# Kernel tuning notes

Hardware: AMD Instinct MI355X
Metric: run time of the kernel (lower is better)

Reference implementation:

```python
import jax, jax.numpy as jnp
import numpy as np

N_E = 1024
E_DIM = 256
N_TOK = 65536
BETA = 0.25


def setup_inputs() -> dict:
    key = jax.random.key(0)
    k1, k2 = jax.random.split(key)
    z = jax.random.normal(k1, (N_TOK, E_DIM), dtype=jnp.float32)
    # nn.Embedding weight, init uniform(-1/n_e, 1/n_e) in the original; use normal-like scale via uniform
    W = jax.random.uniform(k2, (N_E, E_DIM), dtype=jnp.float32, minval=-1.0 / N_E, maxval=1.0 / N_E)
    return {"z": z, "W": W}


def reference(z, W):
    # cosine distance: d = -normalize(z) @ normalize(W).T  -> (N, n_e)
    zn = z / jnp.linalg.norm(z, axis=-1, keepdims=True)
    Wn = W / jnp.linalg.norm(W, axis=-1, keepdims=True)
    d = -jnp.einsum('nd,ed->ne', zn, Wn)
    min_idx = jnp.argmin(d, axis=1)                       # (N,)
    z_q = W[min_idx]                                       # (N, e_dim)
    # commitment / codebook loss with straight-through style detaches
    loss = jnp.mean((jax.lax.stop_gradient(z) - z_q) ** 2) \
         + BETA * jnp.mean((z - jax.lax.stop_gradient(z_q)) ** 2)
    # pos_indices = unique(min_idx) (sorted); neg = np.delete(arange(n_e), pos) (sorted)
    # emb = cat(W[pos], W[neg]); reproduce with a stable argsort on membership mask
    pos_mask = jnp.zeros((N_E,), dtype=bool).at[min_idx].set(True)
    order = jnp.argsort(jnp.logical_not(pos_mask), stable=True)  # pos (sorted) first, then neg (sorted)
    emb = W[order]                                         # (n_e, e_dim)
    label = pos_mask[order].astype(z.dtype)                # (n_e,)
    return emb, label, loss
```

## Files before the change

kernel.cpp:

```cpp
#include <hip/hip_runtime.h>
#include <math.h>


typedef unsigned short u16;
typedef unsigned int   u32;
typedef __attribute__((ext_vector_type(8))) short short8;
typedef __attribute__((ext_vector_type(4))) float f32x4;

#define N_E   1024
#define E_DIM 256
#define N_TOK 65536
#define BETA  0.25f
#define CAP   16
#define D_ADM 0.08f
#define D_FIL 0.09f

#define WS_INVNORM 0
#define WS_MASK    4096
#define WS_LACC    12288
#define WS_WSW     16384
#define WS_CNT     540672
#define WS_CAND    802816

static __device__ __forceinline__ u16 f2bf(float f) {
    u32 u = __float_as_uint(f);
    u32 r = (u + 0x7FFFu + ((u >> 16) & 1u)) >> 16;
    return (u16)r;
}
static __device__ __forceinline__ u32 keyenc(float f) {
    u32 u = __float_as_uint(f);
    return u ^ (u32)(((int)u >> 31) | 0x80000000);
}
static __device__ __forceinline__ float keydec(u32 k) {
    u32 u = (k & 0x80000000u) ? (k ^ 0x80000000u) : ~k;
    return __uint_as_float(u);
}

__global__ void k_prep(const float* __restrict__ W, u16* __restrict__ Wsw,
                       float* __restrict__ inv_norm, int* __restrict__ mask,
                       double* __restrict__ lacc) {
    const int n = blockIdx.x;
    const int l = threadIdx.x;
    const float4 v = reinterpret_cast<const float4*>(W + (size_t)n * E_DIM)[l];
    float s = v.x * v.x + v.y * v.y + v.z * v.z + v.w * v.w;
#pragma unroll
    for (int sh = 1; sh < 64; sh <<= 1) s += __shfl_xor(s, sh, 64);
    const float inv = 1.0f / sqrtf(s);
    if (l == 0) {
        inv_norm[n] = inv;
        mask[n] = 0;
        if (n < 256) lacc[n] = 0.0;
    }
    const int o = l >> 1;
    const int kc = o >> 2, q = o & 3;
    const size_t base =
        (((((size_t)(n >> 7) * 8 + kc) * 8 + ((n >> 4) & 7)) * 64 +
          (q * 16 + (n & 15))) * 8) + (l & 1) * 4;
    u16* dst = Wsw + base;
    dst[0] = f2bf(v.x * inv);
    dst[1] = f2bf(v.y * inv);
    dst[2] = f2bf(v.z * inv);
    dst[3] = f2bf(v.w * inv);
}

__global__ __launch_bounds__(512, 4)
void k_score(const float* __restrict__ z, const u16* __restrict__ Wsw,
             u16* __restrict__ cand_g, u32* __restrict__ cnt_g) {
    __shared__ u16 A_sw[32768];
    __shared__ u32 bestk[128];
    __shared__ u32 cnt[128];
    __shared__ u32 slots[128 * CAP];

    const int t    = threadIdx.x;
    const int lane = t & 63;
    const int w    = t >> 6;
    const int mq2  = w >> 1;
    const int nq   = w & 1;
    const size_t tok_base = (size_t)blockIdx.x * 128;

    if (t < 128) { bestk[t] = 0u; cnt[t] = 0u; }

#pragma unroll
    for (int i = 0; i < 8; i++) {
        const int c = t + 512 * i;
        const int m = c >> 5, o = c & 31;
        const float* zp = z + (tok_base + m) * E_DIM + o * 8;
        const float4 v0 = reinterpret_cast<const float4*>(zp)[0];
        const float4 v1 = reinterpret_cast<const float4*>(zp)[1];
        uint4 d;
        d.x = (u32)f2bf(v0.x) | ((u32)f2bf(v0.y) << 16);
        d.y = (u32)f2bf(v0.z) | ((u32)f2bf(v0.w) << 16);
        d.z = (u32)f2bf(v1.x) | ((u32)f2bf(v1.y) << 16);
        d.w = (u32)f2bf(v1.z) | ((u32)f2bf(v1.w) << 16);
        const int kc = o >> 2, q = o & 3, col = m & 15, mt = m >> 4;
        *reinterpret_cast<uint4*>(A_sw + ((size_t)((kc * 8 + mt) * 64 + q * 16 + col)) * 8) = d;
    }
    __syncthreads();

    const int q   = lane >> 4;
    const int col = lane & 15;
    const u16* wb = Wsw + (size_t)(nq * 4) * 512 + (size_t)lane * 8;

#pragma unroll 1
    for (int nb = 0; nb < 8; nb++) {
        f32x4 acc[2][4];
#pragma unroll
        for (int mi = 0; mi < 2; mi++)
#pragma unroll
            for (int ni = 0; ni < 4; ni++) {
                f32x4 zf = {0.f, 0.f, 0.f, 0.f};
                acc[mi][ni] = zf;
            }

#pragma unroll 2
        for (int kc = 0; kc < 8; kc++) {
            short8 bf[4], af[2];
#pragma unroll
            for (int ni = 0; ni < 4; ni++)
                bf[ni] = *reinterpret_cast<const short8*>(
                    wb + (size_t)(nb * 64 + kc * 8 + ni) * 512);
#pragma unroll
            for (int mi = 0; mi < 2; mi++)
                af[mi] = *reinterpret_cast<const short8*>(
                    A_sw + ((size_t)((kc * 8 + mq2 * 2 + mi) * 64 + lane)) * 8);
#pragma unroll
            for (int mi = 0; mi < 2; mi++)
#pragma unroll
                for (int ni = 0; ni < 4; ni++)
                    acc[mi][ni] = __builtin_amdgcn_mfma_f32_16x16x32_bf16(
                        af[mi], bf[ni], acc[mi][ni], 0, 0, 0);
        }

#pragma unroll
        for (int mi = 0; mi < 2; mi++)
#pragma unroll
            for (int r = 0; r < 4; r++) {
                float m0 = fmaxf(fmaxf(acc[mi][0][r], acc[mi][1][r]),
                                 fmaxf(acc[mi][2][r], acc[mi][3][r]));
#pragma unroll
                for (int sh = 1; sh < 16; sh <<= 1)
                    m0 = fmaxf(m0, __shfl_xor(m0, sh, 64));
                if (col == 0)
                    atomicMax(&bestk[mq2 * 32 + mi * 16 + q * 4 + r], keyenc(m0));
            }
        __syncthreads();

        float thr[8];
#pragma unroll
        for (int mi = 0; mi < 2; mi++)
#pragma unroll
            for (int r = 0; r < 4; r++)
                thr[mi * 4 + r] = keydec(bestk[mq2 * 32 + mi * 16 + q * 4 + r]) - D_ADM;

#pragma unroll
        for (int mi = 0; mi < 2; mi++)
#pragma unroll
            for (int ni = 0; ni < 4; ni++)
#pragma unroll
                for (int r = 0; r < 4; r++) {
                    const float v = acc[mi][ni][r];
                    if (v >= thr[mi * 4 + r]) {
                        const int tok  = mq2 * 32 + mi * 16 + q * 4 + r;
                        const int code = nb * 128 + nq * 64 + ni * 16 + col;
                        const u32 slot = atomicAdd(&cnt[tok], 1u);
                        if (slot < CAP) {
                            const float vc = fminf(fmaxf((v + 16.0f) * 1024.0f, 0.0f), 65535.0f);
                            slots[tok * CAP + slot] = ((u32)vc << 16) | (u32)code;
                        }
                    }
                }
    }

    __syncthreads();
    if (t < 128) {
        const size_t tokg = tok_base + t;
        const u32 c = cnt[t];
        if (c > CAP) {
            cnt_g[tokg] = 0xFFFFFFFFu;
        } else {
            const float thrf = keydec(bestk[t]) - D_FIL;
            u32 m = 0;
            for (u32 i = 0; i < c; i++) {
                const u32 s = slots[t * CAP + i];
                const float approx = (float)(s >> 16) * (1.0f / 1024.0f) - 16.0f;
                if (approx >= thrf) cand_g[tokg * 16 + (m++)] = (u16)(s & 0xFFFFu);
            }
            cnt_g[tokg] = m;
        }
    }
}

__global__ __launch_bounds__(256)
void k_pick(const float* __restrict__ z, const float* __restrict__ W,
            const float* __restrict__ inv_norm, const u16* __restrict__ cand_g,
            const u32* __restrict__ cnt_g, int* __restrict__ mask,
            double* __restrict__ lacc) {
    const int t    = threadIdx.x;
    const int lane = t & 63;
    const int w    = t >> 6;
    const int gl   = t & 15;
    const int grp  = t >> 4;
    const size_t tok = (size_t)blockIdx.x * 16 + grp;

    float4 zv[4];
#pragma unroll
    for (int j = 0; j < 4; j++)
        zv[j] = reinterpret_cast<const float4*>(z + tok * E_DIM)[j * 16 + gl];

    const u32 sc = cnt_g[tok];
    int bi;
    if (sc == 1u) {
        bi = cand_g[tok * 16];
    } else {
        float bv = -3.4e38f;
        bi = 0x7FFFFFFF;
        const bool full = (sc == 0xFFFFFFFFu);
        const int n_it = full ? N_E : (int)sc;
#pragma unroll 1
        for (int i = 0; i < n_it; i++) {
            const int c = full ? i : (int)cand_g[tok * 16 + i];
            float p = 0.f;
#pragma unroll
            for (int j = 0; j < 4; j++) {
                const float4 wv = reinterpret_cast<const float4*>(W + (size_t)c * E_DIM)[j * 16 + gl];
                p += zv[j].x * wv.x + zv[j].y * wv.y + zv[j].z * wv.z + zv[j].w * wv.w;
            }
#pragma unroll
            for (int sh = 1; sh < 16; sh <<= 1) p += __shfl_xor(p, sh, 64);
            const float s = p * inv_norm[c];
            if (s > bv || (s == bv && c < bi)) { bv = s; bi = c; }
        }
    }

    float lsum = 0.f;
#pragma unroll
    for (int j = 0; j < 4; j++) {
        const float4 wv = reinterpret_cast<const float4*>(W + (size_t)bi * E_DIM)[j * 16 + gl];
        const float dx = zv[j].x - wv.x, dy = zv[j].y - wv.y;
        const float dz2 = zv[j].z - wv.z, dw = zv[j].w - wv.w;
        lsum += dx * dx + dy * dy + dz2 * dz2 + dw * dw;
    }
    if (gl == 0) mask[bi] = 1;

#pragma unroll
    for (int sh = 1; sh < 64; sh <<= 1) lsum += __shfl_xor(lsum, sh, 64);
    if (lane == 0) atomicAdd(&lacc[(blockIdx.x * 4 + w) & 255], (double)lsum);
}

__global__ __launch_bounds__(256)
void k_emit(const float* __restrict__ W, const int* __restrict__ mask,
            const double* __restrict__ lacc, float* __restrict__ out) {
    __shared__ int   redp[256], redt[256];
    __shared__ double dred[256];
    const int e = blockIdx.x;
    const int t = threadIdx.x;
    const int4 mv = reinterpret_cast<const int4*>(mask)[t];
    const int b = t * 4;
    redt[t] = mv.x + mv.y + mv.z + mv.w;
    redp[t] = (b + 0 < e ? mv.x : 0) + (b + 1 < e ? mv.y : 0) +
              (b + 2 < e ? mv.z : 0) + (b + 3 < e ? mv.w : 0);
    if (e == 0) dred[t] = lacc[t];
    __syncthreads();
#pragma unroll
    for (int s2 = 128; s2 > 0; s2 >>= 1) {
        if (t < s2) {
            redp[t] += redp[t + s2];
            redt[t] += redt[t + s2];
            if (e == 0) dred[t] += dred[t + s2];
        }
        __syncthreads();
    }
    const int prefix = redp[0], total = redt[0];
    const int m = mask[e];
    const int r = m ? prefix : (total + e - prefix);
    out[(size_t)r * E_DIM + t] = W[(size_t)e * E_DIM + t];
    if (t == 0) out[(size_t)N_E * E_DIM + r] = m ? 1.0f : 0.0f;
    if (e == 0 && t == 0) {
        const double mse = dred[0] / (double)((size_t)N_TOK * E_DIM);
        out[(size_t)N_E * E_DIM + N_E] = (float)((1.0 + (double)BETA) * mse);
    }
}

extern "C" void kernel_launch(void* const* d_in, const int* in_sizes, int n_in,
                              void* d_out, int out_size, void* d_ws, size_t ws_size,
                              hipStream_t stream) {
    const float* z = (const float*)d_in[0];
    const float* W = (const float*)d_in[1];
    float* out = (float*)d_out;
    char* ws = (char*)d_ws;

    float*  inv_norm = (float*)(ws + WS_INVNORM);
    int*    mask     = (int*)(ws + WS_MASK);
    double* lacc     = (double*)(ws + WS_LACC);
    u16*    Wsw      = (u16*)(ws + WS_WSW);
    u32*    cnt      = (u32*)(ws + WS_CNT);
    u16*    cand     = (u16*)(ws + WS_CAND);

    k_prep <<<N_E, 64, 0, stream>>>(W, Wsw, inv_norm, mask, lacc);
    k_score<<<N_TOK / 128, 512, 0, stream>>>(z, Wsw, cand, cnt);
    k_pick <<<N_TOK / 16, 256, 0, stream>>>(z, W, inv_norm, cand, cnt, mask, lacc);
    k_emit <<<N_E, 256, 0, stream>>>(W, mask, lacc, out);
}
```

Baseline: 161.8 us.

## Resolve unambiguous tokens in score kernel and compact ambiguous ones for pick

The score kernel now accumulates ||z||^2 during the bf16 staging and, when a token has a single surviving candidate, derives its squared-error term algebraically from the best cosine score and ||W|| while setting the mask directly. Only ambiguous tokens are appended to a compacted worklist, and a small persistent pick kernel processes that list. This removes the full second pass over z and W for most tokens. The MFMA loop is also restructured into a 4x2 tile with software-pipelined double-buffered fragment loads, and score quantisation is made finer. The loss now relies on a bf16-derived best score (approx error) and uses a smaller global candidate cap.

Measured after the change: 541.8 us. 235% more time.

```diff
diff --git a/kernel.cpp b/kernel.cpp
--- a/kernel.cpp
+++ b/kernel.cpp
@@ -4,6 +4,7 @@
 
 typedef unsigned short u16;
 typedef unsigned int   u32;
+typedef unsigned long long u64;
 typedef __attribute__((ext_vector_type(8))) short short8;
 typedef __attribute__((ext_vector_type(4))) float f32x4;
 
@@ -11,21 +12,24 @@
 #define E_DIM 256
 #define N_TOK 65536
 #define BETA  0.25f
-#define CAP   16
+#define CAPL  16
+#define CAPG  8
 #define D_ADM 0.08f
 #define D_FIL 0.09f
 
 #define WS_INVNORM 0
-#define WS_MASK    4096
+#define WS_NORMW   4096
+#define WS_MASK    8192
 #define WS_LACC    12288
+#define WS_WCNT    14336
 #define WS_WSW     16384
 #define WS_CNT     540672
 #define WS_CAND    802816
+#define WS_WLIST   1851392
 
 static __device__ __forceinline__ u16 f2bf(float f) {
     u32 u = __float_as_uint(f);
-    u32 r = (u + 0x7FFFu + ((u >> 16) & 1u)) >> 16;
-    return (u16)r;
+    return (u16)((u + 0x7FFFu + ((u >> 16) & 1u)) >> 16);
 }
 static __device__ __forceinline__ u32 keyenc(float f) {
     u32 u = __float_as_uint(f);
@@ -37,19 +41,20 @@
 }
 
 __global__ void k_prep(const float* __restrict__ W, u16* __restrict__ Wsw,
-                       float* __restrict__ inv_norm, int* __restrict__ mask,
-                       double* __restrict__ lacc) {
+                       float* __restrict__ inv_norm, float* __restrict__ normW,
+                       int* __restrict__ mask, double* __restrict__ lacc,
+                       u32* __restrict__ wcnt) {
     const int n = blockIdx.x;
     const int l = threadIdx.x;
     const float4 v = reinterpret_cast<const float4*>(W + (size_t)n * E_DIM)[l];
     float s = v.x * v.x + v.y * v.y + v.z * v.z + v.w * v.w;
 #pragma unroll
     for (int sh = 1; sh < 64; sh <<= 1) s += __shfl_xor(s, sh, 64);
-    const float inv = 1.0f / sqrtf(s);
+    const float nw = sqrtf(s), inv = 1.0f / nw;
     if (l == 0) {
-        inv_norm[n] = inv;
-        mask[n] = 0;
+        inv_norm[n] = inv; normW[n] = nw; mask[n] = 0;
         if (n < 256) lacc[n] = 0.0;
+        if (n == 0) *wcnt = 0u;
     }
     const int o = l >> 1;
     const int kc = o >> 2, q = o & 3;
@@ -65,160 +70,183 @@
 
 __global__ __launch_bounds__(512, 4)
 void k_score(const float* __restrict__ z, const u16* __restrict__ Wsw,
-             u16* __restrict__ cand_g, u32* __restrict__ cnt_g) {
-    __shared__ u16 A_sw[32768];
+             const float* __restrict__ normW, u16* __restrict__ cand_g,
+             u32* __restrict__ cnt_g, int* __restrict__ mask,
+             u32* __restrict__ wlist, u32* __restrict__ wcnt,
+             double* __restrict__ lacc) {
+    __shared__ __align__(16) u16 A_sw[32768];
     __shared__ u32 bestk[128];
     __shared__ u32 cnt[128];
-    __shared__ u32 slots[128 * CAP];
+    __shared__ u32 slots[128 * CAPL];
 
     const int t    = threadIdx.x;
     const int lane = t & 63;
     const int w    = t >> 6;
-    const int mq2  = w >> 1;
-    const int nq   = w & 1;
     const size_t tok_base = (size_t)blockIdx.x * 128;
 
     if (t < 128) { bestk[t] = 0u; cnt[t] = 0u; }
 
-#pragma unroll
-    for (int i = 0; i < 8; i++) {
-        const int c = t + 512 * i;
-        const int m = c >> 5, o = c & 31;
-        const float* zp = z + (tok_base + m) * E_DIM + o * 8;
-        const float4 v0 = reinterpret_cast<const float4*>(zp)[0];
-        const float4 v1 = reinterpret_cast<const float4*>(zp)[1];
-        uint4 d;
-        d.x = (u32)f2bf(v0.x) | ((u32)f2bf(v0.y) << 16);
-        d.y = (u32)f2bf(v0.z) | ((u32)f2bf(v0.w) << 16);
-        d.z = (u32)f2bf(v1.x) | ((u32)f2bf(v1.y) << 16);
-        d.w = (u32)f2bf(v1.z) | ((u32)f2bf(v1.w) << 16);
-        const int kc = o >> 2, q = o & 3, col = m & 15, mt = m >> 4;
-        *reinterpret_cast<uint4*>(A_sw + ((size_t)((kc * 8 + mt) * 64 + q * 16 + col)) * 8) = d;
-    }
+    float ssq = 0.f;
+    {
+        const int col16 = lane & 15, oq = lane >> 4;
+#pragma unroll
+        for (int i = 0; i < 8; i++) {
+            const int f  = i * 8 + w;
+            const int kc = f >> 3, mt = f & 7;
+            const int m  = mt * 16 + col16;
+            const int o  = kc * 4 + oq;
+            const float* zp = z + (tok_base + m) * E_DIM + o * 8;
+            const float4 v0 = reinterpret_cast<const float4*>(zp)[0];
+            const float4 v1 = reinterpret_cast<const float4*>(zp)[1];
+            ssq += v0.x * v0.x + v0.y * v0.y + v0.z * v0.z + v0.w * v0.w
+                 + v1.x * v1.x + v1.y * v1.y + v1.z * v1.z + v1.w * v1.w;
+            uint4 d;
+            d.x = (u32)f2bf(v0.x) | ((u32)f2bf(v0.y) << 16);
+            d.y = (u32)f2bf(v0.z) | ((u32)f2bf(v0.w) << 16);
+            d.z = (u32)f2bf(v1.x) | ((u32)f2bf(v1.y) << 16);
+            d.w = (u32)f2bf(v1.z) | ((u32)f2bf(v1.w) << 16);
+            *reinterpret_cast<uint4*>(A_sw + (size_t)f * 512 + (size_t)lane * 8) = d;
+        }
+    }
+#pragma unroll
+    for (int sh = 1; sh < 64; sh <<= 1) ssq += __shfl_xor(ssq, sh, 64);
+    if (lane == 0) atomicAdd(&lacc[(blockIdx.x * 8 + w) & 255], (double)ssq);
     __syncthreads();
 
-    const int q   = lane >> 4;
-    const int col = lane & 15;
-    const u16* wb = Wsw + (size_t)(nq * 4) * 512 + (size_t)lane * 8;
-
-#pragma unroll 1
-    for (int nb = 0; nb < 8; nb++) {
-        f32x4 acc[2][4];
-#pragma unroll
-        for (int mi = 0; mi < 2; mi++)
-#pragma unroll
-            for (int ni = 0; ni < 4; ni++) {
-                f32x4 zf = {0.f, 0.f, 0.f, 0.f};
-                acc[mi][ni] = zf;
-            }
-
-#pragma unroll 2
-        for (int kc = 0; kc < 8; kc++) {
-            short8 bf[4], af[2];
-#pragma unroll
-            for (int ni = 0; ni < 4; ni++)
-                bf[ni] = *reinterpret_cast<const short8*>(
-                    wb + (size_t)(nb * 64 + kc * 8 + ni) * 512);
-#pragma unroll
-            for (int mi = 0; mi < 2; mi++)
-                af[mi] = *reinterpret_cast<const short8*>(
-                    A_sw + ((size_t)((kc * 8 + mq2 * 2 + mi) * 64 + lane)) * 8);
-#pragma unroll
-            for (int mi = 0; mi < 2; mi++)
-#pragma unroll
-                for (int ni = 0; ni < 4; ni++)
-                    acc[mi][ni] = __builtin_amdgcn_mfma_f32_16x16x32_bf16(
-                        af[mi], bf[ni], acc[mi][ni], 0, 0, 0);
-        }
-
-#pragma unroll
-        for (int mi = 0; mi < 2; mi++)
-#pragma unroll
-            for (int r = 0; r < 4; r++) {
-                float m0 = fmaxf(fmaxf(acc[mi][0][r], acc[mi][1][r]),
-                                 fmaxf(acc[mi][2][r], acc[mi][3][r]));
-#pragma unroll
-                for (int sh = 1; sh < 16; sh <<= 1)
-                    m0 = fmaxf(m0, __shfl_xor(m0, sh, 64));
-                if (col == 0)
-                    atomicMax(&bestk[mq2 * 32 + mi * 16 + q * 4 + r], keyenc(m0));
-            }
-        __syncthreads();
-
-        float thr[8];
-#pragma unroll
-        for (int mi = 0; mi < 2; mi++)
-#pragma unroll
-            for (int r = 0; r < 4; r++)
-                thr[mi * 4 + r] = keydec(bestk[mq2 * 32 + mi * 16 + q * 4 + r]) - D_ADM;
-
-#pragma unroll
-        for (int mi = 0; mi < 2; mi++)
-#pragma unroll
-            for (int ni = 0; ni < 4; ni++)
+    const int mq = w >> 2;
+    const int nq = w & 3;
+    const int q = lane >> 4, col = lane & 15;
+    const u16* wbase = Wsw + (size_t)(nq * 2) * 512 + (size_t)lane * 8;
+
+    f32x4 acc[4][2];
+#pragma unroll
+    for (int mi = 0; mi < 4; mi++)
+#pragma unroll
+        for (int ni = 0; ni < 2; ni++) {
+            f32x4 zf = {0.f, 0.f, 0.f, 0.f};
+            acc[mi][ni] = zf;
+        }
+
+#define LOAD_B(S, D) { \
+    D[0] = *reinterpret_cast<const short8*>(wbase + (size_t)((S) * 8 + 0) * 512); \
+    D[1] = *reinterpret_cast<const short8*>(wbase + (size_t)((S) * 8 + 1) * 512); }
+#define LOAD_A(S, D) { const int _k8 = ((S) & 7) * 8; \
+    D[0] = *reinterpret_cast<const short8*>(A_sw + (size_t)(_k8 + mq * 4 + 0) * 512 + (size_t)lane * 8); \
+    D[1] = *reinterpret_cast<const short8*>(A_sw + (size_t)(_k8 + mq * 4 + 1) * 512 + (size_t)lane * 8); \
+    D[2] = *reinterpret_cast<const short8*>(A_sw + (size_t)(_k8 + mq * 4 + 2) * 512 + (size_t)lane * 8); \
+    D[3] = *reinterpret_cast<const short8*>(A_sw + (size_t)(_k8 + mq * 4 + 3) * 512 + (size_t)lane * 8); }
+#define MFMA_STEP(AF, BF) { \
+    _Pragma("unroll") for (int mi = 0; mi < 4; mi++) \
+    _Pragma("unroll") for (int ni = 0; ni < 2; ni++) \
+        acc[mi][ni] = __builtin_amdgcn_mfma_f32_16x16x32_bf16(AF[mi], BF[ni], acc[mi][ni], 0, 0, 0); }
+
+    short8 afc[4], bfc[2], afn[4], bfn[2];
+    LOAD_B(0, bfc); LOAD_A(0, afc);
+
+#pragma unroll 4
+    for (int s = 0; s < 64; s += 2) {
+        LOAD_B(s + 1, bfn); LOAD_A(s + 1, afn);
+        MFMA_STEP(afc, bfc);
+        if (s < 62) { LOAD_B(s + 2, bfc); LOAD_A(s + 2, afc); }
+        MFMA_STEP(afn, bfn);
+        if (((s + 1) & 7) == 7) {
+            const int nb = (s + 1) >> 3;
+#pragma unroll
+            for (int mi = 0; mi < 4; mi++)
 #pragma unroll
                 for (int r = 0; r < 4; r++) {
-                    const float v = acc[mi][ni][r];
-                    if (v >= thr[mi * 4 + r]) {
-                        const int tok  = mq2 * 32 + mi * 16 + q * 4 + r;
-                        const int code = nb * 128 + nq * 64 + ni * 16 + col;
-                        const u32 slot = atomicAdd(&cnt[tok], 1u);
-                        if (slot < CAP) {
-                            const float vc = fminf(fmaxf((v + 16.0f) * 1024.0f, 0.0f), 65535.0f);
-                            slots[tok * CAP + slot] = ((u32)vc << 16) | (u32)code;
+                    float m0 = fmaxf(acc[mi][0][r], acc[mi][1][r]);
+#pragma unroll
+                    for (int sh = 1; sh < 16; sh <<= 1)
+                        m0 = fmaxf(m0, __shfl_xor(m0, sh, 64));
+                    const int tk = mq * 64 + mi * 16 + q * 4 + r;
+                    if (col == 0) atomicMax(&bestk[tk], keyenc(m0));
+                    const float thr = fmaxf(m0, keydec(bestk[tk])) - D_ADM;
+#pragma unroll
+                    for (int ni = 0; ni < 2; ni++) {
+                        const float v = acc[mi][ni][r];
+                        if (v >= thr) {
+                            const int code = nb * 128 + nq * 32 + ni * 16 + col;
+                            const u32 sl = atomicAdd(&cnt[tk], 1u);
+                            if (sl < CAPL) {
+                                const float vc = fminf(fmaxf((v + 16.f) * 2048.f, 0.f), 65535.f);
+                                slots[tk * CAPL + sl] = ((u32)vc << 16) | (u32)code;
+                            }
                         }
+                        acc[mi][ni][r] = 0.f;
                     }
                 }
-    }
+        }
+    }
+#undef LOAD_B
+#undef LOAD_A
+#undef MFMA_STEP
 
     __syncthreads();
     if (t < 128) {
         const size_t tokg = tok_base + t;
         const u32 c = cnt[t];
-        if (c > CAP) {
-            cnt_g[tokg] = 0xFFFFFFFFu;
+        const float best = keydec(bestk[t]);
+        bool amb = false;
+        float xacc = 0.f;
+        if (c > CAPL) {
+            cnt_g[tokg] = 0xFFFFFFFFu; amb = true;
         } else {
-            const float thrf = keydec(bestk[t]) - D_FIL;
-            u32 m = 0;
+            const float thrf = best - D_FIL;
+            u16 loc[CAPG]; u32 m = 0;
             for (u32 i = 0; i < c; i++) {
-                const u32 s = slots[t * CAP + i];
-                const float approx = (float)(s >> 16) * (1.0f / 1024.0f) - 16.0f;
-                if (approx >= thrf) cand_g[tokg * 16 + (m++)] = (u16)(s & 0xFFFFu);
+                const u32 s2 = slots[t * CAPL + i];
+                const float ap = (float)(s2 >> 16) * (1.0f / 2048.0f) - 16.0f;
+                if (ap >= thrf) { if (m < CAPG) loc[m] = (u16)(s2 & 0xFFFFu); m++; }
             }
-            cnt_g[tokg] = m;
-        }
+            if (m == 1) {
+                const int bi = loc[0];
+                mask[bi] = 1;
+                const float nw = normW[bi];
+                xacc = fmaf(-2.0f * best, nw, nw * nw);
+            } else if (m <= CAPG) {
+                for (u32 i = 0; i < m; i++) cand_g[tokg * CAPG + i] = loc[i];
+                cnt_g[tokg] = m; amb = true;
+            } else {
+                cnt_g[tokg] = 0xFFFFFFFFu; amb = true;
+            }
+        }
+        const u64 bal = __ballot(amb);
+        u32 base = 0;
+        if (lane == 0) base = atomicAdd(wcnt, (u32)__popcll(bal));
+        base = (u32)__shfl((int)base, 0, 64);
+        if (amb) wlist[base + (u32)__popcll(bal & ((1ull << lane) - 1ull))] = (u32)tokg;
+        float xs = xacc;
+#pragma unroll
+        for (int sh = 1; sh < 64; sh <<= 1) xs += __shfl_xor(xs, sh, 64);
+        if (lane == 0) atomicAdd(&lacc[(blockIdx.x * 2 + w) & 255], (double)xs);
     }
 }
 
 __global__ __launch_bounds__(256)
 void k_pick(const float* __restrict__ z, const float* __restrict__ W,
-            const float* __restrict__ inv_norm, const u16* __restrict__ cand_g,
-            const u32* __restrict__ cnt_g, int* __restrict__ mask,
-            double* __restrict__ lacc) {
-    const int t    = threadIdx.x;
-    const int lane = t & 63;
-    const int w    = t >> 6;
-    const int gl   = t & 15;
-    const int grp  = t >> 4;
-    const size_t tok = (size_t)blockIdx.x * 16 + grp;
-
-    float4 zv[4];
-#pragma unroll
-    for (int j = 0; j < 4; j++)
-        zv[j] = reinterpret_cast<const float4*>(z + tok * E_DIM)[j * 16 + gl];
-
-    const u32 sc = cnt_g[tok];
-    int bi;
-    if (sc == 1u) {
-        bi = cand_g[tok * 16];
-    } else {
-        float bv = -3.4e38f;
-        bi = 0x7FFFFFFF;
+            const float* __restrict__ inv_norm, const float* __restrict__ normW,
+            const u16* __restrict__ cand_g, const u32* __restrict__ cnt_g,
+            const u32* __restrict__ wlist, const u32* __restrict__ wcnt,
+            int* __restrict__ mask, double* __restrict__ lacc) {
+    const int t = threadIdx.x, lane = t & 63;
+    const int gl = t & 15, grp = t >> 4;
+    const u32 total = *wcnt;
+    float xs = 0.f;
+    for (u32 i = blockIdx.x * 16 + grp; i < total; i += 128 * 16) {
+        const size_t tok = wlist[i];
+        float4 zv[4];
+#pragma unroll
+        for (int j = 0; j < 4; j++)
+            zv[j] = reinterpret_cast<const float4*>(z + tok * E_DIM)[j * 16 + gl];
+        const u32 sc = cnt_g[tok];
         const bool full = (sc == 0xFFFFFFFFu);
         const int n_it = full ? N_E : (int)sc;
+        float bv = -3.4e38f, bp = 0.f;
+        int bi = 0x7FFFFFFF;
 #pragma unroll 1
-        for (int i = 0; i < n_it; i++) {
-            const int c = full ? i : (int)cand_g[tok * 16 + i];
+        for (int k2 = 0; k2 < n_it; k2++) {
+            const int c = full ? k2 : (int)cand_g[tok * CAPG + k2];
             float p = 0.f;
 #pragma unroll
             for (int j = 0; j < 4; j++) {
@@ -228,29 +256,22 @@
 #pragma unroll
             for (int sh = 1; sh < 16; sh <<= 1) p += __shfl_xor(p, sh, 64);
             const float s = p * inv_norm[c];
-            if (s > bv || (s == bv && c < bi)) { bv = s; bi = c; }
-        }
-    }
-
-    float lsum = 0.f;
-#pragma unroll
-    for (int j = 0; j < 4; j++) {
-        const float4 wv = reinterpret_cast<const float4*>(W + (size_t)bi * E_DIM)[j * 16 + gl];
-        const float dx = zv[j].x - wv.x, dy = zv[j].y - wv.y;
-        const float dz2 = zv[j].z - wv.z, dw = zv[j].w - wv.w;
-        lsum += dx * dx + dy * dy + dz2 * dz2 + dw * dw;
-    }
-    if (gl == 0) mask[bi] = 1;
-
-#pragma unroll
-    for (int sh = 1; sh < 64; sh <<= 1) lsum += __shfl_xor(lsum, sh, 64);
-    if (lane == 0) atomicAdd(&lacc[(blockIdx.x * 4 + w) & 255], (double)lsum);
+            if (s > bv || (s == bv && c < bi)) { bv = s; bi = c; bp = p; }
+        }
+        if (gl == 0) {
+            mask[bi] = 1;
+            xs += fmaf(-2.0f, bp, normW[bi] * normW[bi]);
+        }
+    }
+    xs += __shfl_xor(xs, 16, 64);
+    xs += __shfl_xor(xs, 32, 64);
+    if (lane == 0) atomicAdd(&lacc[(blockIdx.x * 4 + (t >> 6)) & 255], (double)xs);
 }
 
 __global__ __launch_bounds__(256)
 void k_emit(const float* __restrict__ W, const int* __restrict__ mask,
             const double* __restrict__ lacc, float* __restrict__ out) {
-    __shared__ int   redp[256], redt[256];
+    __shared__ int    redp[256], redt[256];
     __shared__ double dred[256];
     const int e = blockIdx.x;
     const int t = threadIdx.x;
@@ -290,14 +311,19 @@
     char* ws = (char*)d_ws;
 
     float*  inv_norm = (float*)(ws + WS_INVNORM);
+    float*  normW    = (float*)(ws + WS_NORMW);
     int*    mask     = (int*)(ws + WS_MASK);
     double* lacc     = (double*)(ws + WS_LACC);
+    u32*    wcnt     = (u32*)(ws + WS_WCNT);
     u16*    Wsw      = (u16*)(ws + WS_WSW);
     u32*    cnt      = (u32*)(ws + WS_CNT);
     u16*    cand     = (u16*)(ws + WS_CAND);
-
-    k_prep <<<N_E, 64, 0, stream>>>(W, Wsw, inv_norm, mask, lacc);
-    k_score<<<N_TOK / 128, 512, 0, stream>>>(z, Wsw, cand, cnt);
-    k_pick <<<N_TOK / 16, 256, 0, stream>>>(z, W, inv_norm, cand, cnt, mask, lacc);
+    u32*    wlist    = (u32*)(ws + WS_WLIST);
+
+    k_prep <<<N_E, 64, 0, stream>>>(W, Wsw, inv_norm, normW, mask, lacc, wcnt);
+    k_score<<<N_TOK / 128, 512, 0, stream>>>(z, Wsw, normW, cand, cnt, mask,
+                                             wlist, wcnt, lacc);
+    k_pick <<<128, 256, 0, stream>>>(z, W, inv_norm, normW, cand, cnt,
+                                     wlist, wcnt, mask, lacc);
     k_emit <<<N_E, 256, 0, stream>>>(W, mask, lacc, out);
 }
```
